# Optimization experiments

Measured on AMD Instinct MI355X. Metric: run time of the kernel, lower is better.

## Reference

```python
import jax, jax.numpy as jnp
import numpy as np

D_MODEL = 256; N_HEADS = 8; N_LEVELS = 4; N_POINTS = 4; D_FF = 2048
SHAPES = [(128, 128), (64, 64), (32, 32), (16, 16)]  # (H_l, W_l) per level
LV = sum(h * w for h, w in SHAPES)  # 21760
B = 8; NQ = 900
EPS = 1e-5


def layer_norm(x, s, b):
    m = x.mean(-1, keepdims=True)
    v = x.var(-1, keepdims=True)
    return (x - m) * jax.lax.rsqrt(v + EPS) * s + b


def mha(q, k, v, in_w, in_b, out_w, out_b):
    # torch nn.MultiheadAttention, batch_first, eval mode (no dropout)
    Bq, Lq, C = q.shape
    h = N_HEADS; d = C // h
    wq, wk, wv = jnp.split(in_w, 3, axis=0)
    bq, bk, bv = jnp.split(in_b, 3)
    qh = (q @ wq.T + bq).reshape(Bq, Lq, h, d)
    kh = (k @ wk.T + bk).reshape(Bq, -1, h, d)
    vh = (v @ wv.T + bv).reshape(Bq, -1, h, d)
    scale = jnp.asarray(1.0 / np.sqrt(d), q.dtype)
    attn = jax.nn.softmax(jnp.einsum('bqhd,bkhd->bhqk', qh, kh) * scale, axis=-1)
    o = jnp.einsum('bhqk,bkhd->bqhd', attn, vh).reshape(Bq, Lq, C)
    return o @ out_w.T + out_b


def deform_attn(query, ref, memory, spatial_shapes, val_w, val_b, off_w, off_b, aw_w, aw_b, co_w, co_b):
    # MSDeformAttn forward (eval): offsets/weights from query, bilinear sample value per level/point
    Bq, Lq, C = query.shape
    h, L, P = N_HEADS, N_LEVELS, N_POINTS
    dh = C // h
    value = (memory @ val_w.T + val_b).reshape(Bq, -1, h, dh)  # (B, Lv, h, dh)
    off = (query @ off_w.T + off_b).reshape(Bq, Lq, h, L, P, 2)
    aw = jax.nn.softmax((query @ aw_w.T + aw_b).reshape(Bq, Lq, h, L * P), axis=-1)
    aw = aw.reshape(Bq, Lq, h, L, P)
    # normalizer = (W_l, H_l) per level
    normalizer = spatial_shapes[:, ::-1].astype(query.dtype)
    loc = ref[:, :, None, :, None, :] + off / normalizer[None, None, None, :, None, :]  # (B,Lq,h,L,P,2)
    out = jnp.zeros((Bq, h, Lq, dh), query.dtype)
    start = 0
    for l, (Hl, Wl) in enumerate(SHAPES):
        v_l = value[:, start:start + Hl * Wl].transpose(0, 2, 1, 3)  # (B,h,Hl*Wl,dh)
        start += Hl * Wl
        xy = loc[:, :, :, l]  # (B,Lq,h,P,2) normalized in [0,1]
        # grid_sample align_corners=False pixel coords
        x = xy[..., 0] * Wl - 0.5
        y = xy[..., 1] * Hl - 0.5
        x0 = jnp.floor(x); y0 = jnp.floor(y)
        wx = x - x0; wy = y - y0
        acc = jnp.zeros((Bq, h, Lq * P, dh), query.dtype)
        for dx, dy, w in ((0, 0, (1 - wx) * (1 - wy)), (1, 0, wx * (1 - wy)),
                          (0, 1, (1 - wx) * wy), (1, 1, wx * wy)):
            xi = x0 + dx; yi = y0 + dy
            valid = (xi >= 0) & (xi <= Wl - 1) & (yi >= 0) & (yi <= Hl - 1)
            xi = jnp.clip(xi, 0, Wl - 1).astype(jnp.int32)
            yi = jnp.clip(yi, 0, Hl - 1).astype(jnp.int32)
            idx = (yi * Wl + xi).transpose(0, 2, 1, 3).reshape(Bq, h, Lq * P)
            g = jnp.take_along_axis(v_l, idx[..., None], axis=2)  # (B,h,Lq*P,dh)
            wgt = (w * valid).transpose(0, 2, 1, 3).reshape(Bq, h, Lq * P)
            acc = acc + g * wgt[..., None]
        acc = acc.reshape(Bq, h, Lq, P, dh)
        wl = aw[:, :, :, l].transpose(0, 2, 1, 3)  # (B,h,Lq,P)
        out = out + jnp.einsum('bhqpd,bhqp->bhqd', acc, wl)
    out = out.transpose(0, 2, 1, 3).reshape(Bq, Lq, C)
    return out @ co_w.T + co_b


def forward(tgt, memory, query_pos, reference_points, sa_in_w, sa_in_b, sa_out_w, sa_out_b,
            off_w, off_b, aw_w, aw_b, val_w, val_b, co_w, co_b,
            l1_w, l1_b, l2_w, l2_b, ln1_s, ln1_b, ln2_s, ln2_b, ln3_s, ln3_b, spatial_shapes):
    q = tgt + query_pos  # with_pos_embed; eval mode: no group_detr split, no dropout
    tgt2 = mha(q, q, tgt, sa_in_w, sa_in_b, sa_out_w, sa_out_b)
    tgt = layer_norm(tgt + tgt2, ln1_s, ln1_b)
    tgt2 = deform_attn(tgt + query_pos, reference_points, memory, spatial_shapes,
                       val_w, val_b, off_w, off_b, aw_w, aw_b, co_w, co_b)
    tgt = layer_norm(tgt + tgt2, ln2_s, ln2_b)
    tgt2 = jax.nn.relu(tgt @ l1_w.T + l1_b) @ l2_w.T + l2_b
    return layer_norm(tgt + tgt2, ln3_s, ln3_b)


def setup_inputs():
    key = jax.random.key(0)
    ks = jax.random.split(key, 16)
    C = D_MODEL
    f = lambda i, shape, s=0.02: jax.random.normal(ks[i], shape, jnp.float32) * s
    HLP = N_HEADS * N_LEVELS * N_POINTS
    return {
        'tgt': f(0, (B, NQ, C), 1.0),
        'memory': f(1, (B, LV, C), 1.0),
        'query_pos': f(2, (B, NQ, C), 1.0),
        'reference_points': jax.random.uniform(ks[3], (B, NQ, N_LEVELS, 2), jnp.float32),
        'sa_in_w': f(4, (3 * C, C)), 'sa_in_b': jnp.zeros((3 * C,), jnp.float32),
        'sa_out_w': f(5, (C, C)), 'sa_out_b': jnp.zeros((C,), jnp.float32),
        'off_w': f(6, (HLP * 2, C)), 'off_b': f(7, (HLP * 2,), 0.5),
        'aw_w': f(8, (HLP, C)), 'aw_b': jnp.zeros((HLP,), jnp.float32),
        'val_w': f(9, (C, C)), 'val_b': jnp.zeros((C,), jnp.float32),
        'co_w': f(10, (C, C)), 'co_b': jnp.zeros((C,), jnp.float32),
        'l1_w': f(11, (D_FF, C)), 'l1_b': jnp.zeros((D_FF,), jnp.float32),
        'l2_w': f(12, (C, D_FF)), 'l2_b': jnp.zeros((C,), jnp.float32),
        'ln1_s': jnp.ones((C,), jnp.float32), 'ln1_b': jnp.zeros((C,), jnp.float32),
        'ln2_s': jnp.ones((C,), jnp.float32), 'ln2_b': jnp.zeros((C,), jnp.float32),
        'ln3_s': jnp.ones((C,), jnp.float32), 'ln3_b': jnp.zeros((C,), jnp.float32),
        'spatial_shapes': jnp.asarray(SHAPES, jnp.int32),
        'level_start_index': jnp.asarray(np.cumsum([0] + [h * w for h, w in SHAPES[:-1]]), jnp.int32),
    }


def reference(tgt, memory, query_pos, reference_points, sa_in_w, sa_in_b, sa_out_w, sa_out_b,
              off_w, off_b, aw_w, aw_b, val_w, val_b, co_w, co_b,
              l1_w, l1_b, l2_w, l2_b, ln1_s, ln1_b, ln2_s, ln2_b, ln3_s, ln3_b,
              spatial_shapes, level_start_index):
    return forward(tgt, memory, query_pos, reference_points, sa_in_w, sa_in_b, sa_out_w, sa_out_b,
                   off_w, off_b, aw_w, aw_b, val_w, val_b, co_w, co_b,
                   l1_w, l1_b, l2_w, l2_b, ln1_s, ln1_b, ln2_s, ln2_b, ln3_s, ln3_b, spatial_shapes)
```

## Files before the change

kernel.cpp:

```cpp
#include <hip/hip_runtime.h>
#include <hip/hip_bf16.h>

#define NQL 900
#define CDIM 256
#define BDIM 8
#define LVTOT 21760

typedef __bf16 bf16x8 __attribute__((ext_vector_type(8)));
typedef float f32x4 __attribute__((ext_vector_type(4)));
typedef uint u32x4 __attribute__((ext_vector_type(4)));
typedef uint u32x2 __attribute__((ext_vector_type(2)));

__device__ __forceinline__ ushort f2bf(float x) {
  uint u = __builtin_bit_cast(uint, x);
  u += 0x7fff + ((u >> 16) & 1);
  return (ushort)(u >> 16);
}

template <bool ABF16, bool AADD, bool RELU, bool OUTBF16>
__global__ __launch_bounds__(256, 4) void mgemm_kernel(const void* __restrict__ Ap,
                                                       const float* __restrict__ A2p,
                                                       const float* __restrict__ W,
                                                       const float* __restrict__ bias,
                                                       void* __restrict__ Cout,
                                                       int M, int N, int K) {
  __shared__ ushort smem[10240];
  ushort* As = smem;
  ushort* Bs = smem + 5120;
  const int tid = threadIdx.x;
  const int m0 = blockIdx.y * 128, n0 = blockIdx.x * 128;
  const int wv = tid >> 6;
  const int wm = (wv >> 1) * 64, wn = (wv & 1) * 64;
  const int lane = tid & 63;
  const int lr = lane & 15, kq = lane >> 4;

  f32x4 acc[4][4] = {};
  float4 pa[2][2], pb[2][2];
  u32x4 pa16[2];

  auto load_tiles = [&](int k0) {
#pragma unroll
    for (int it = 0; it < 2; ++it) {
      int idx = it * 256 + tid;
      int r = idx >> 2, s = (idx & 3) << 3;
      int gm = min(m0 + r, M - 1);
      if constexpr (ABF16) {
        pa16[it] = *(const u32x4*)((const ushort*)Ap + (size_t)gm * K + k0 + s);
      } else {
        const float* ap = (const float*)Ap + (size_t)gm * K + k0 + s;
        pa[it][0] = *(const float4*)ap;
        pa[it][1] = *(const float4*)(ap + 4);
        if constexpr (AADD) {
          const float* ap2 = A2p + (size_t)gm * K + k0 + s;
          float4 q0 = *(const float4*)ap2;
          float4 q1 = *(const float4*)(ap2 + 4);
          pa[it][0].x += q0.x; pa[it][0].y += q0.y; pa[it][0].z += q0.z; pa[it][0].w += q0.w;
          pa[it][1].x += q1.x; pa[it][1].y += q1.y; pa[it][1].z += q1.z; pa[it][1].w += q1.w;
        }
      }
      int gn = min(n0 + r, N - 1);
      const float* wp = W + (size_t)gn * K + k0 + s;
      pb[it][0] = *(const float4*)wp;
      pb[it][1] = *(const float4*)(wp + 4);
    }
  };

  auto store_tiles = [&]() {
#pragma unroll
    for (int it = 0; it < 2; ++it) {
      int idx = it * 256 + tid;
      int r = idx >> 2, s = (idx & 3) << 3;
      u32x4 u;
      if constexpr (ABF16) {
        u = pa16[it];
      } else {
        u.x = f2bf(pa[it][0].x) | ((uint)f2bf(pa[it][0].y) << 16);
        u.y = f2bf(pa[it][0].z) | ((uint)f2bf(pa[it][0].w) << 16);
        u.z = f2bf(pa[it][1].x) | ((uint)f2bf(pa[it][1].y) << 16);
        u.w = f2bf(pa[it][1].z) | ((uint)f2bf(pa[it][1].w) << 16);
      }
      *(u32x4*)&As[r * 40 + s] = u;
      u32x4 w;
      w.x = f2bf(pb[it][0].x) | ((uint)f2bf(pb[it][0].y) << 16);
      w.y = f2bf(pb[it][0].z) | ((uint)f2bf(pb[it][0].w) << 16);
      w.z = f2bf(pb[it][1].x) | ((uint)f2bf(pb[it][1].y) << 16);
      w.w = f2bf(pb[it][1].z) | ((uint)f2bf(pb[it][1].w) << 16);
      *(u32x4*)&Bs[r * 40 + s] = w;
    }
  };

  load_tiles(0);
  for (int k0 = 0; k0 < K; k0 += 32) {
    store_tiles();
    __syncthreads();
    if (k0 + 32 < K) load_tiles(k0 + 32);
    bf16x8 af[4], bq[4];
#pragma unroll
    for (int m = 0; m < 4; ++m)
      af[m] = __builtin_bit_cast(bf16x8, *(const u32x4*)&As[(wm + m * 16 + lr) * 40 + kq * 8]);
#pragma unroll
    for (int n = 0; n < 4; ++n)
      bq[n] = __builtin_bit_cast(bf16x8, *(const u32x4*)&Bs[(wn + n * 16 + lr) * 40 + kq * 8]);
#pragma unroll
    for (int m = 0; m < 4; ++m)
#pragma unroll
      for (int n = 0; n < 4; ++n)
        acc[m][n] = __builtin_amdgcn_mfma_f32_16x16x32_bf16(af[m], bq[n], acc[m][n], 0, 0, 0);
    __syncthreads();
  }

  if constexpr (OUTBF16) {
    ushort* Cs = smem;
#pragma unroll
    for (int p = 0; p < 2; ++p) {
      __syncthreads();
      if (wm == p * 64) {
#pragma unroll
        for (int n = 0; n < 4; ++n) {
          int col = wn + n * 16 + lr;
          float bv = bias[n0 + col];
#pragma unroll
          for (int m = 0; m < 4; ++m)
#pragma unroll
            for (int j = 0; j < 4; ++j) {
              float v = acc[m][n][j] + bv;
              if (RELU) v = fmaxf(v, 0.f);
              Cs[(m * 16 + kq * 4 + j) * 136 + col] = f2bf(v);
            }
        }
      }
      __syncthreads();
#pragma unroll
      for (int it = 0; it < 4; ++it) {
        int idx = it * 256 + tid;
        int r = idx >> 4, c = (idx & 15) * 8;
        int grow = m0 + p * 64 + r;
        if (grow < M) {
          u32x4 u = *(const u32x4*)&Cs[r * 136 + c];
          *(u32x4*)((ushort*)Cout + (size_t)grow * N + n0 + c) = u;
        }
      }
    }
  } else {
#pragma unroll
    for (int n = 0; n < 4; ++n) {
      int gcol = n0 + wn + n * 16 + lr;
      float bv = bias[gcol];
#pragma unroll
      for (int m = 0; m < 4; ++m) {
        int rbase = m0 + wm + m * 16 + kq * 4;
#pragma unroll
        for (int j = 0; j < 4; ++j) {
          int grow = rbase + j;
          if (grow >= M) continue;
          float v = acc[m][n][j] + bv;
          if (RELU) v = fmaxf(v, 0.f);
          ((float*)Cout)[(size_t)grow * N + gcol] = v;
        }
      }
    }
  }
}

template <bool ABF16, bool AADD, bool RELU, bool HASRES, bool DOSM, bool OUTBF16>
__global__ __launch_bounds__(256, 4) void mgemm64_kernel(const void* __restrict__ Ap,
                                                         const float* __restrict__ A2p,
                                                         const float* __restrict__ W,
                                                         const float* __restrict__ bias,
                                                         const float* __restrict__ Rres,
                                                         void* __restrict__ Cout,
                                                         int M, int N, int K) {
  __shared__ ushort smem[5120];
  ushort* As = smem;
  ushort* Bs = smem + 2560;
  const int tid = threadIdx.x;
  const int m0 = blockIdx.y * 64, n0 = blockIdx.x * 64;
  const int wv = tid >> 6, lane = tid & 63;
  const int wm = (wv >> 1) * 32, wn = (wv & 1) * 32;
  const int lr = lane & 15, kq = lane >> 4;

  f32x4 acc[2][2] = {};
  float4 pa[2], pb[2];
  u32x4 pa16;

  auto load_tiles = [&](int k0) {
    int r = tid >> 2, s = (tid & 3) << 3;
    int gm = min(m0 + r, M - 1);
    if constexpr (ABF16) {
      pa16 = *(const u32x4*)((const ushort*)Ap + (size_t)gm * K + k0 + s);
    } else {
      const float* ap = (const float*)Ap + (size_t)gm * K + k0 + s;
      pa[0] = *(const float4*)ap;
      pa[1] = *(const float4*)(ap + 4);
      if constexpr (AADD) {
        const float* ap2 = A2p + (size_t)gm * K + k0 + s;
        float4 q0 = *(const float4*)ap2;
        float4 q1 = *(const float4*)(ap2 + 4);
        pa[0].x += q0.x; pa[0].y += q0.y; pa[0].z += q0.z; pa[0].w += q0.w;
        pa[1].x += q1.x; pa[1].y += q1.y; pa[1].z += q1.z; pa[1].w += q1.w;
      }
    }
    int gn = min(n0 + r, N - 1);
    const float* wp = W + (size_t)gn * K + k0 + s;
    pb[0] = *(const float4*)wp;
    pb[1] = *(const float4*)(wp + 4);
  };

  auto store_tiles = [&]() {
    int r = tid >> 2, s = (tid & 3) << 3;
    u32x4 u;
    if constexpr (ABF16) {
      u = pa16;
    } else {
      u.x = f2bf(pa[0].x) | ((uint)f2bf(pa[0].y) << 16);
      u.y = f2bf(pa[0].z) | ((uint)f2bf(pa[0].w) << 16);
      u.z = f2bf(pa[1].x) | ((uint)f2bf(pa[1].y) << 16);
      u.w = f2bf(pa[1].z) | ((uint)f2bf(pa[1].w) << 16);
    }
    *(u32x4*)&As[r * 40 + s] = u;
    u32x4 w;
    w.x = f2bf(pb[0].x) | ((uint)f2bf(pb[0].y) << 16);
    w.y = f2bf(pb[0].z) | ((uint)f2bf(pb[0].w) << 16);
    w.z = f2bf(pb[1].x) | ((uint)f2bf(pb[1].y) << 16);
    w.w = f2bf(pb[1].z) | ((uint)f2bf(pb[1].w) << 16);
    *(u32x4*)&Bs[r * 40 + s] = w;
  };

  load_tiles(0);
  for (int k0 = 0; k0 < K; k0 += 32) {
    store_tiles();
    __syncthreads();
    if (k0 + 32 < K) load_tiles(k0 + 32);
    bf16x8 af[2], bq[2];
#pragma unroll
    for (int m = 0; m < 2; ++m)
      af[m] = __builtin_bit_cast(bf16x8, *(const u32x4*)&As[(wm + m * 16 + lr) * 40 + kq * 8]);
#pragma unroll
    for (int n = 0; n < 2; ++n)
      bq[n] = __builtin_bit_cast(bf16x8, *(const u32x4*)&Bs[(wn + n * 16 + lr) * 40 + kq * 8]);
#pragma unroll
    for (int m = 0; m < 2; ++m)
#pragma unroll
      for (int n = 0; n < 2; ++n)
        acc[m][n] = __builtin_amdgcn_mfma_f32_16x16x32_bf16(af[m], bq[n], acc[m][n], 0, 0, 0);
    __syncthreads();
  }

  if constexpr (OUTBF16) {
    ushort* Cs = smem;
    __syncthreads();
#pragma unroll
    for (int n = 0; n < 2; ++n) {
      int col = wn + n * 16 + lr;
      float bv = bias[n0 + col];
#pragma unroll
      for (int m = 0; m < 2; ++m)
#pragma unroll
        for (int j = 0; j < 4; ++j) {
          float v = acc[m][n][j] + bv;
          if (RELU) v = fmaxf(v, 0.f);
          Cs[(wm + m * 16 + kq * 4 + j) * 72 + col] = f2bf(v);
        }
    }
    __syncthreads();
#pragma unroll
    for (int it = 0; it < 2; ++it) {
      int idx = it * 256 + tid;
      int r = idx >> 3, c = (idx & 7) * 8;
      int grow = m0 + r;
      if (grow < M) {
        u32x4 u = *(const u32x4*)&Cs[r * 72 + c];
        *(u32x4*)((ushort*)Cout + (size_t)grow * N + n0 + c) = u;
      }
    }
  } else {
#pragma unroll
    for (int n = 0; n < 2; ++n) {
      int gcol = n0 + wn + n * 16 + lr;
      float bv = bias[gcol];
#pragma unroll
      for (int m = 0; m < 2; ++m) {
        int rbase = m0 + wm + m * 16 + kq * 4;
#pragma unroll
        for (int j = 0; j < 4; ++j) {
          int grow = rbase + j;
          float v = acc[m][n][j] + bv;
          if constexpr (DOSM) {
            float gmax = v;
#pragma unroll
            for (int w = 1; w < 16; w <<= 1) gmax = fmaxf(gmax, __shfl_xor(gmax, w));
            float e = __expf(v - gmax);
            float gs = e;
#pragma unroll
            for (int w = 1; w < 16; w <<= 1) gs += __shfl_xor(gs, w);
            v = e / gs;
          }
          if (grow >= M) continue;
          if (HASRES) v += Rres[(size_t)grow * N + gcol];
          if (RELU) v = fmaxf(v, 0.f);
          ((float*)Cout)[(size_t)grow * N + gcol] = v;
        }
      }
    }
  }
}

__global__ __launch_bounds__(256) void wconv_kernel(const float* __restrict__ W,
                                                    ushort* __restrict__ Wbf) {
  int idx = (blockIdx.x * 256 + threadIdx.x) * 4;
  float4 v = *(const float4*)(W + idx);
  u32x2 u;
  u.x = f2bf(v.x) | ((uint)f2bf(v.y) << 16);
  u.y = f2bf(v.z) | ((uint)f2bf(v.w) << 16);
  *(u32x2*)(Wbf + idx) = u;
}

__global__ __launch_bounds__(256, 4) void vproj_kernel(const float* __restrict__ A,
                                                       const ushort* __restrict__ Wbf,
                                                       const float* __restrict__ bias,
                                                       ushort* __restrict__ Cout) {
  __shared__ ushort As[64 * 264];
  const int tid = threadIdx.x;
  const int m0 = blockIdx.x * 64;
  const int wv = tid >> 6, lane = tid & 63;
  const int lr = lane & 15, kq = lane >> 4;

  {
    const float* base = A + (size_t)m0 * 256;
    float4 v[16];
#pragma unroll
    for (int it = 0; it < 16; ++it)
      v[it] = *(const float4*)(base + (size_t)(it * 256 + tid) * 4);
#pragma unroll
    for (int it = 0; it < 16; ++it) {
      int f4 = it * 256 + tid;
      int row = f4 >> 6;
      int col = (f4 & 63) * 4;
      u32x2 w;
      w.x = f2bf(v[it].x) | ((uint)f2bf(v[it].y) << 16);
      w.y = f2bf(v[it].z) | ((uint)f2bf(v[it].w) << 16);
      *(u32x2*)&As[row * 264 + col] = w;
    }
  }
  __syncthreads();

  const ushort* wbase = Wbf + (size_t)(wv * 64 + lr) * 256 + kq * 8;
  f32x4 acc[4][4] = {};
#pragma unroll
  for (int k0 = 0; k0 < 256; k0 += 32) {
    u32x4 bw[4];
#pragma unroll
    for (int ng = 0; ng < 4; ++ng)
      bw[ng] = *(const u32x4*)(wbase + ng * 16 * 256 + k0);
    bf16x8 af[4];
#pragma unroll
    for (int m = 0; m < 4; ++m)
      af[m] = __builtin_bit_cast(bf16x8, *(const u32x4*)&As[(m * 16 + lr) * 264 + k0 + kq * 8]);
#pragma unroll
    for (int m = 0; m < 4; ++m)
#pragma unroll
      for (int ng = 0; ng < 4; ++ng)
        acc[m][ng] = __builtin_amdgcn_mfma_f32_16x16x32_bf16(
            af[m], __builtin_bit_cast(bf16x8, bw[ng]), acc[m][ng], 0, 0, 0);
  }
  __syncthreads();

  ushort* Cs = As;
#pragma unroll
  for (int ng = 0; ng < 4; ++ng) {
    int col = wv * 64 + ng * 16 + lr;
    float bv = bias[col];
#pragma unroll
    for (int m = 0; m < 4; ++m)
#pragma unroll
      for (int j = 0; j < 4; ++j)
        Cs[(m * 16 + kq * 4 + j) * 264 + col] = f2bf(acc[m][ng][j] + bv);
  }
  __syncthreads();
#pragma unroll
  for (int it = 0; it < 8; ++it) {
    int idx = it * 256 + tid;
    int r = idx >> 5, c = (idx & 31) * 8;
    u32x4 u = *(const u32x4*)&Cs[r * 264 + c];
    *(u32x4*)(Cout + (size_t)(m0 + r) * 256 + c) = u;
  }
}

__global__ __launch_bounds__(256) void vt_kernel(const ushort* __restrict__ tmp_v,
                                                 ushort* __restrict__ vt) {
  __shared__ ushort Ls[64 * 40];
  const int qt = blockIdx.x;
  const int bh = blockIdx.y;
  const int b = bh >> 3, h = bh & 7;
  const int tid = threadIdx.x;
  const int q0 = qt * 64;
  {
    int r = tid >> 2, c = (tid & 3) * 8;
    int gq = min(q0 + r, NQL - 1);
    u32x4 u = *(const u32x4*)(tmp_v + ((size_t)(b * NQL + gq) * 256) + h * 32 + c);
    *(u32x4*)&Ls[r * 40 + c] = u;
  }
  __syncthreads();
  {
    int d = tid >> 3, qw = (tid & 7) * 8;
    u32x4 u;
    uint w[8];
#pragma unroll
    for (int j = 0; j < 8; ++j) w[j] = Ls[(qw + j) * 40 + d];
    u.x = w[0] | (w[1] << 16);
    u.y = w[2] | (w[3] << 16);
    u.z = w[4] | (w[5] << 16);
    u.w = w[6] | (w[7] << 16);
    *(u32x4*)(vt + ((size_t)(bh * 32 + d) * 960) + q0 + qw) = u;
  }
}

__global__ __launch_bounds__(256, 2) void fattn_kernel(const ushort* __restrict__ qk,
                                                       const ushort* __restrict__ vt,
                                                       float* __restrict__ out) {
  __shared__ ushort Ks[64 * 40];
  __shared__ ushort Vs[32 * 72];
  __shared__ ushort Ps[4][16 * 72];
  const int qt = blockIdx.x, bh = blockIdx.y;
  const int b = bh >> 3, h = bh & 7;
  const int tid = threadIdx.x;
  const int wv = tid >> 6, lane = tid & 63;
  const int lq = lane & 15, hi = lane >> 4;
  const int q0 = qt * 64 + wv * 16;
  const float SC = 0.17677669529663689f;

  bf16x8 qfrag;
  {
    int qrow = min(q0 + lq, NQL - 1);
    qfrag = __builtin_bit_cast(bf16x8,
        *(const u32x4*)(qk + (size_t)(b * NQL + qrow) * 512 + h * 32 + hi * 8));
  }

  f32x4 o0 = {}, o1 = {};
  float mrow = -1e30f, lrow = 0.f;

  for (int kt = 0; kt < 15; ++kt) {
    const int k0 = kt * 64;
    __syncthreads();
    {
      int r = tid >> 2, c = (tid & 3) * 8;
      int gk = min(k0 + r, NQL - 1);
      u32x4 u = *(const u32x4*)(qk + (size_t)(b * NQL + gk) * 512 + 256 + h * 32 + c);
      *(u32x4*)&Ks[r * 40 + c] = u;
    }
    {
      int r = tid >> 3, c = (tid & 7) * 8;
      u32x4 u = *(const u32x4*)(vt + (size_t)(bh * 32 + r) * 960 + k0 + c);
      *(u32x4*)&Vs[r * 72 + c] = u;
    }
    __syncthreads();

    f32x4 st[4];
#pragma unroll
    for (int mt = 0; mt < 4; ++mt) {
      bf16x8 kf = __builtin_bit_cast(bf16x8, *(const u32x4*)&Ks[(mt * 16 + lq) * 40 + hi * 8]);
      f32x4 z = {};
      st[mt] = __builtin_amdgcn_mfma_f32_16x16x32_bf16(kf, qfrag, z, 0, 0, 0);
    }
    float sv[4][4];
    float lmax = -1e30f;
#pragma unroll
    for (int mt = 0; mt < 4; ++mt)
#pragma unroll
      for (int j = 0; j < 4; ++j) {
        int key = k0 + mt * 16 + hi * 4 + j;
        float v = st[mt][j] * SC;
        v = (key < NQL) ? v : -1e30f;
        sv[mt][j] = v;
        lmax = fmaxf(lmax, v);
      }
    lmax = fmaxf(lmax, __shfl_xor(lmax, 16));
    lmax = fmaxf(lmax, __shfl_xor(lmax, 32));
    float mnew = fmaxf(mrow, lmax);
    float rs = __expf(mrow - mnew);
    float lsum = 0.f;
    uint pw[4][2];
#pragma unroll
    for (int mt = 0; mt < 4; ++mt) {
      float p0 = __expf(sv[mt][0] - mnew);
      float p1 = __expf(sv[mt][1] - mnew);
      float p2 = __expf(sv[mt][2] - mnew);
      float p3 = __expf(sv[mt][3] - mnew);
      lsum += (p0 + p1) + (p2 + p3);
      pw[mt][0] = f2bf(p0) | ((uint)f2bf(p1) << 16);
      pw[mt][1] = f2bf(p2) | ((uint)f2bf(p3) << 16);
    }
    lsum += __shfl_xor(lsum, 16);
    lsum += __shfl_xor(lsum, 32);
    lrow = lrow * rs + lsum;
    mrow = mnew;
#pragma unroll
    for (int j = 0; j < 4; ++j) {
      float rsj = __shfl(rs, hi * 4 + j);
      o0[j] *= rsj;
      o1[j] *= rsj;
    }
#pragma unroll
    for (int mt = 0; mt < 4; ++mt) {
      u32x2 u;
      u.x = pw[mt][0];
      u.y = pw[mt][1];
      *(u32x2*)&Ps[wv][lq * 72 + mt * 16 + hi * 4] = u;
    }
#pragma unroll
    for (int k2 = 0; k2 < 2; ++k2) {
      bf16x8 pa = __builtin_bit_cast(bf16x8, *(const u32x4*)&Ps[wv][lq * 72 + k2 * 32 + hi * 8]);
      bf16x8 vb0 = __builtin_bit_cast(bf16x8, *(const u32x4*)&Vs[(0 * 16 + lq) * 72 + k2 * 32 + hi * 8]);
      bf16x8 vb1 = __builtin_bit_cast(bf16x8, *(const u32x4*)&Vs[(1 * 16 + lq) * 72 + k2 * 32 + hi * 8]);
      o0 = __builtin_amdgcn_mfma_f32_16x16x32_bf16(pa, vb0, o0, 0, 0, 0);
      o1 = __builtin_amdgcn_mfma_f32_16x16x32_bf16(pa, vb1, o1, 0, 0, 0);
    }
  }

#pragma unroll
  for (int j = 0; j < 4; ++j) {
    float lj = __shfl(lrow, hi * 4 + j);
    float inv = 1.f / lj;
    int gq = q0 + hi * 4 + j;
    if (gq < NQL) {
      float* op = out + (size_t)(b * NQL + gq) * 256 + h * 32;
      op[lq] = o0[j] * inv;
      op[16 + lq] = o1[j] * inv;
    }
  }
}

__global__ __launch_bounds__(256) void ln_kernel(const float* __restrict__ x,
                                                 const float* __restrict__ s,
                                                 const float* __restrict__ bb,
                                                 float* __restrict__ out, int M) {
  const int wv = threadIdx.x >> 6, lane = threadIdx.x & 63;
  const int row = blockIdx.x * 4 + wv;
  if (row >= M) return;
  const float4 v = *(const float4*)(x + (size_t)row * 256 + lane * 4);
  float s1 = (v.x + v.y) + (v.z + v.w);
  float s2 = (v.x * v.x + v.y * v.y) + (v.z * v.z + v.w * v.w);
#pragma unroll
  for (int w = 1; w < 64; w <<= 1) {
    s1 += __shfl_xor(s1, w);
    s2 += __shfl_xor(s2, w);
  }
  float mean = s1 * (1.f / 256.f);
  float var = s2 * (1.f / 256.f) - mean * mean;
  float inv = rsqrtf(var + 1e-5f);
  float4 sc = *(const float4*)(s + lane * 4);
  float4 bv = *(const float4*)(bb + lane * 4);
  float4 o;
  o.x = (v.x - mean) * inv * sc.x + bv.x;
  o.y = (v.y - mean) * inv * sc.y + bv.y;
  o.z = (v.z - mean) * inv * sc.z + bv.z;
  o.w = (v.w - mean) * inv * sc.w + bv.w;
  *(float4*)(out + (size_t)row * 256 + lane * 4) = o;
}

__global__ __launch_bounds__(256) void deform_kernel(const __hip_bfloat16* __restrict__ value,
                                                     const float* __restrict__ offb,
                                                     const float* __restrict__ awb,
                                                     const float* __restrict__ refp,
                                                     float* __restrict__ dfout) {
  const int Hs[4] = {128, 64, 32, 16};
  const int Stl[4] = {0, 16384, 20480, 21504};
  int row = blockIdx.x;
  int b = row / NQL;
  int tid = threadIdx.x;
  int h = tid >> 5, d = tid & 31;
  const float* off = offb + (size_t)row * 256;
  const float* aw = awb + (size_t)row * 128;
  const float* ref = refp + (size_t)row * 8;
  const __hip_bfloat16* vb = value + (size_t)b * LVTOT * 256 + h * 32 + d;
  float acc = 0.f;
#pragma unroll
  for (int l = 0; l < 4; ++l) {
    int Wi = Hs[l], Hi = Hs[l];
    float Wl = (float)Wi, Hl = (float)Hi;
    int st = Stl[l];
    float rx = ref[l * 2 + 0], ry = ref[l * 2 + 1];
#pragma unroll
    for (int p = 0; p < 4; ++p) {
      int oi = ((h * 4 + l) * 4 + p) * 2;
      float x = (rx + off[oi] / Wl) * Wl - 0.5f;
      float y = (ry + off[oi + 1] / Hl) * Hl - 0.5f;
      float w = aw[h * 16 + l * 4 + p];
      float x0f = floorf(x), y0f = floorf(y);
      float wx = x - x0f, wy = y - y0f;
      int xi0 = (int)x0f, yi0 = (int)y0f;
      float samp = 0.f;
#pragma unroll
      for (int dy = 0; dy < 2; ++dy) {
#pragma unroll
        for (int dx = 0; dx < 2; ++dx) {
          int xi = xi0 + dx, yi = yi0 + dy;
          float tw = (dx ? wx : 1.f - wx) * (dy ? wy : 1.f - wy);
          bool valid = (xi >= 0) && (xi < Wi) && (yi >= 0) && (yi < Hi);
          int xc = min(max(xi, 0), Wi - 1);
          int yc = min(max(yi, 0), Hi - 1);
          float vv = __bfloat162float(vb[(size_t)(st + yc * Wi + xc) * 256]);
          samp += valid ? tw * vv : 0.f;
        }
      }
      acc = fmaf(w, samp, acc);
    }
  }
  dfout[(size_t)row * 256 + tid] = acc;
}

extern "C" void kernel_launch(void* const* d_in, const int* in_sizes, int n_in,
                              void* d_out, int out_size, void* d_ws, size_t ws_size,
                              hipStream_t stream) {
  const float* tgt = (const float*)d_in[0];
  const float* memory = (const float*)d_in[1];
  const float* qpos = (const float*)d_in[2];
  const float* refp = (const float*)d_in[3];
  const float* sa_in_w = (const float*)d_in[4];
  const float* sa_in_b = (const float*)d_in[5];
  const float* sa_out_w = (const float*)d_in[6];
  const float* sa_out_b = (const float*)d_in[7];
  const float* off_w = (const float*)d_in[8];
  const float* off_b = (const float*)d_in[9];
  const float* aw_w = (const float*)d_in[10];
  const float* aw_b = (const float*)d_in[11];
  const float* val_w = (const float*)d_in[12];
  const float* val_b = (const float*)d_in[13];
  const float* co_w = (const float*)d_in[14];
  const float* co_b = (const float*)d_in[15];
  const float* l1_w = (const float*)d_in[16];
  const float* l1_b = (const float*)d_in[17];
  const float* l2_w = (const float*)d_in[18];
  const float* l2_b = (const float*)d_in[19];
  const float* ln1_s = (const float*)d_in[20];
  const float* ln1_b = (const float*)d_in[21];
  const float* ln2_s = (const float*)d_in[22];
  const float* ln2_b = (const float*)d_in[23];
  const float* ln3_s = (const float*)d_in[24];
  const float* ln3_b = (const float*)d_in[25];

  float* ws = (float*)d_ws;
  const size_t E = (size_t)BDIM * NQL * CDIM;
  ushort* vt = (ushort*)(ws + E);
  float* attn_o = ws + 4 * E;
  ushort* tmp_qk = (ushort*)(ws + 5 * E);
  ushort* tmp_v = (ushort*)(ws + 7 * E);
  float* sa_out = ws + 5 * E;
  float* offb = ws + E;
  float* awb = ws + 2 * E;
  float* dfout = ws + 3 * E;
  float* co_out = ws + 4 * E;
  ushort* hidden = (ushort*)ws;
  float* ffn_o = ws + 4 * E;
  float* tgt1 = ws + 8 * E;
  float* tgt2 = ws + 9 * E;
  ushort* wbf = (ushort*)(ws + 10 * E);
  ushort* valbf = (ushort*)(ws + 11 * E);

  const int M = BDIM * NQL;
  const int MT = (M + 127) / 128;
  const int M64 = (M + 63) / 64;
  const int LNG = (M + 3) / 4;
  dim3 blk(256);

  wconv_kernel<<<64, blk, 0, stream>>>(val_w, wbf);
  mgemm64_kernel<false, true, false, false, false, true><<<dim3(8, M64), blk, 0, stream>>>(
      tgt, qpos, sa_in_w, sa_in_b, nullptr, tmp_qk, M, 512, 256);
  mgemm64_kernel<false, false, false, false, false, true><<<dim3(4, M64), blk, 0, stream>>>(
      tgt, nullptr, sa_in_w + 512 * 256, sa_in_b + 512, nullptr, tmp_v, M, 256, 256);
  vt_kernel<<<dim3(15, 64), blk, 0, stream>>>(tmp_v, vt);
  fattn_kernel<<<dim3(15, 64), blk, 0, stream>>>(tmp_qk, vt, attn_o);
  mgemm64_kernel<false, false, false, true, false, false><<<dim3(4, M64), blk, 0, stream>>>(
      attn_o, nullptr, sa_out_w, sa_out_b, tgt, sa_out, M, 256, 256);
  ln_kernel<<<LNG, blk, 0, stream>>>(sa_out, ln1_s, ln1_b, tgt1, M);
  vproj_kernel<<<(BDIM * LVTOT) / 64, blk, 0, stream>>>(memory, wbf, val_b, valbf);
  mgemm64_kernel<false, true, false, false, false, false><<<dim3(4, M64), blk, 0, stream>>>(
      tgt1, qpos, off_w, off_b, nullptr, offb, M, 256, 256);
  mgemm64_kernel<false, true, false, false, true, false><<<dim3(2, M64), blk, 0, stream>>>(
      tgt1, qpos, aw_w, aw_b, nullptr, awb, M, 128, 256);
  deform_kernel<<<M, blk, 0, stream>>>((const __hip_bfloat16*)valbf, offb, awb, refp, dfout);
  mgemm64_kernel<false, false, false, true, false, false><<<dim3(4, M64), blk, 0, stream>>>(
      dfout, nullptr, co_w, co_b, tgt1, co_out, M, 256, 256);
  ln_kernel<<<LNG, blk, 0, stream>>>(co_out, ln2_s, ln2_b, tgt2, M);
  mgemm_kernel<false, false, true, true><<<dim3(16, MT), blk, 0, stream>>>(
      tgt2, nullptr, l1_w, l1_b, hidden, M, 2048, 256);
  mgemm64_kernel<true, false, false, true, false, false><<<dim3(4, M64), blk, 0, stream>>>(
      hidden, nullptr, l2_w, l2_b, tgt2, ffn_o, M, 256, 2048);
  ln_kernel<<<LNG, blk, 0, stream>>>(ffn_o, ln3_s, ln3_b, (float*)d_out, M);
}
```

Before: 341.4 us.

## Restructure value projection so each wave computes a full 16-row slab from registers

The value projection kernel no longer stages a 64x256 fp32 tile into shared memory with block-wide barriers. Each wave now owns a 16-row slab across all 256 output columns. It loads its A rows straight from global memory into registers, converts them to bf16 with software prefetch of the next K chunk, and reads every weight column directly from global or L2. This removes the block-level syncs and the shared-memory A staging, but each wave now re-reads the whole weight matrix and holds 16 accumulators plus 16 bias registers, which raises register pressure and weight traffic.

```diff
diff --git a/kernel.cpp b/kernel.cpp
--- a/kernel.cpp
+++ b/kernel.cpp
@@ -15,6 +15,15 @@
   uint u = __builtin_bit_cast(uint, x);
   u += 0x7fff + ((u >> 16) & 1);
   return (ushort)(u >> 16);
+}
+
+__device__ __forceinline__ bf16x8 pack8(const float4& a, const float4& b) {
+  u32x4 u;
+  u.x = f2bf(a.x) | ((uint)f2bf(a.y) << 16);
+  u.y = f2bf(a.z) | ((uint)f2bf(a.w) << 16);
+  u.z = f2bf(b.x) | ((uint)f2bf(b.y) << 16);
+  u.w = f2bf(b.z) | ((uint)f2bf(b.w) << 16);
+  return __builtin_bit_cast(bf16x8, u);
 }
 
 template <bool ABF16, bool AADD, bool RELU, bool OUTBF16>
@@ -319,70 +328,71 @@
                                                        const ushort* __restrict__ Wbf,
                                                        const float* __restrict__ bias,
                                                        ushort* __restrict__ Cout) {
-  __shared__ ushort As[64 * 264];
+  __shared__ ushort Cs[4][16 * 264];
   const int tid = threadIdx.x;
-  const int m0 = blockIdx.x * 64;
   const int wv = tid >> 6, lane = tid & 63;
   const int lr = lane & 15, kq = lane >> 4;
-
-  {
-    const float* base = A + (size_t)m0 * 256;
-    float4 v[16];
-#pragma unroll
-    for (int it = 0; it < 16; ++it)
-      v[it] = *(const float4*)(base + (size_t)(it * 256 + tid) * 4);
-#pragma unroll
-    for (int it = 0; it < 16; ++it) {
-      int f4 = it * 256 + tid;
-      int row = f4 >> 6;
-      int col = (f4 & 63) * 4;
-      u32x2 w;
-      w.x = f2bf(v[it].x) | ((uint)f2bf(v[it].y) << 16);
-      w.y = f2bf(v[it].z) | ((uint)f2bf(v[it].w) << 16);
-      *(u32x2*)&As[row * 264 + col] = w;
-    }
-  }
-  __syncthreads();
-
-  const ushort* wbase = Wbf + (size_t)(wv * 64 + lr) * 256 + kq * 8;
-  f32x4 acc[4][4] = {};
-#pragma unroll
-  for (int k0 = 0; k0 < 256; k0 += 32) {
-    u32x4 bw[4];
-#pragma unroll
-    for (int ng = 0; ng < 4; ++ng)
-      bw[ng] = *(const u32x4*)(wbase + ng * 16 * 256 + k0);
-    bf16x8 af[4];
-#pragma unroll
-    for (int m = 0; m < 4; ++m)
-      af[m] = __builtin_bit_cast(bf16x8, *(const u32x4*)&As[(m * 16 + lr) * 264 + k0 + kq * 8]);
-#pragma unroll
-    for (int m = 0; m < 4; ++m)
-#pragma unroll
-      for (int ng = 0; ng < 4; ++ng)
-        acc[m][ng] = __builtin_amdgcn_mfma_f32_16x16x32_bf16(
-            af[m], __builtin_bit_cast(bf16x8, bw[ng]), acc[m][ng], 0, 0, 0);
-  }
-  __syncthreads();
-
-  ushort* Cs = As;
+  const int slab = blockIdx.x * 4 + wv;
+  const float* arow = A + (size_t)(slab * 16 + lr) * 256 + kq * 8;
+  const ushort* wb = Wbf + (size_t)lr * 256 + kq * 8;
+
+  float bv[16];
 #pragma unroll
   for (int ng = 0; ng < 4; ++ng) {
-    int col = wv * 64 + ng * 16 + lr;
-    float bv = bias[col];
-#pragma unroll
-    for (int m = 0; m < 4; ++m)
-#pragma unroll
-      for (int j = 0; j < 4; ++j)
-        Cs[(m * 16 + kq * 4 + j) * 264 + col] = f2bf(acc[m][ng][j] + bv);
-  }
-  __syncthreads();
+    bv[ng] = bias[ng * 16 + lr];
+  }
+#pragma unroll
+  for (int ng = 4; ng < 16; ++ng) bv[ng] = bias[ng * 16 + lr];
+
+  f32x4 acc[16] = {};
+  float4 va[2][4];
+
+#pragma unroll
+  for (int j = 0; j < 2; ++j) {
+    va[j][0] = *(const float4*)(arow + 32 * j);
+    va[j][1] = *(const float4*)(arow + 32 * j + 4);
+  }
+
+#pragma unroll
+  for (int jp = 0; jp < 4; ++jp) {
+    bf16x8 af0 = pack8(va[0][0], va[0][1]);
+    bf16x8 af1 = pack8(va[1][0], va[1][1]);
+    if (jp < 3) {
+#pragma unroll
+      for (int j = 0; j < 2; ++j) {
+        int jn = (jp + 1) * 2 + j;
+        va[j][0] = *(const float4*)(arow + 32 * jn);
+        va[j][1] = *(const float4*)(arow + 32 * jn + 4);
+      }
+    }
+    const ushort* w0 = wb + (size_t)(jp * 2) * 32;
+    const ushort* w1 = wb + (size_t)(jp * 2 + 1) * 32;
+#pragma unroll
+    for (int ng = 0; ng < 16; ++ng) {
+      bf16x8 bw0 = __builtin_bit_cast(bf16x8, *(const u32x4*)(w0 + (size_t)ng * 4096));
+      acc[ng] = __builtin_amdgcn_mfma_f32_16x16x32_bf16(af0, bw0, acc[ng], 0, 0, 0);
+    }
+#pragma unroll
+    for (int ng = 0; ng < 16; ++ng) {
+      bf16x8 bw1 = __builtin_bit_cast(bf16x8, *(const u32x4*)(w1 + (size_t)ng * 4096));
+      acc[ng] = __builtin_amdgcn_mfma_f32_16x16x32_bf16(af1, bw1, acc[ng], 0, 0, 0);
+    }
+  }
+
+  ushort* cs = Cs[wv];
+#pragma unroll
+  for (int ng = 0; ng < 16; ++ng) {
+#pragma unroll
+    for (int j = 0; j < 4; ++j)
+      cs[(kq * 4 + j) * 264 + ng * 16 + lr] = f2bf(acc[ng][j] + bv[ng]);
+  }
+  ushort* cb = Cout + (size_t)slab * 16 * 256;
 #pragma unroll
   for (int it = 0; it < 8; ++it) {
-    int idx = it * 256 + tid;
-    int r = idx >> 5, c = (idx & 31) * 8;
-    u32x4 u = *(const u32x4*)&Cs[r * 264 + c];
-    *(u32x4*)(Cout + (size_t)(m0 + r) * 256 + c) = u;
+    int row = it * 2 + (lane >> 5);
+    int c = (lane & 31) * 8;
+    u32x4 u = *(const u32x4*)&cs[row * 264 + c];
+    *(u32x4*)(cb + (size_t)row * 256 + c) = u;
   }
 }
 
```

After: 489.3 us. 43.3% more time.
